# Kernel tuning notes

Measured on AMD Instinct MI355X. Metric: run time of the kernel, lower is better.

## Reference

```python
import jax, jax.numpy as jnp
import numpy as np

DIST_THRESH = 150.0
ROW_EPS = 1e-6
BN_EPS = 1e-5


def setup_inputs() -> dict:
    key = jax.random.key(0)
    ks = jax.random.split(key, 6)
    B, N, T, D = 64, 64, 16, 512
    person_features = jax.random.normal(ks[0], (B, N, T, D), dtype=jnp.float32)
    # bboxes in pixel-ish units so the 150px threshold gives a mixed adjacency
    bboxes = jax.random.uniform(ks[1], (B, N, 4), dtype=jnp.float32) * 300.0
    w1 = jax.random.normal(ks[2], (D, D), dtype=jnp.float32) * (1.0 / np.sqrt(D))
    b1 = jax.random.normal(ks[3], (D,), dtype=jnp.float32) * 0.02
    w2 = jax.random.normal(ks[4], (D, D), dtype=jnp.float32) * (1.0 / np.sqrt(D))
    b2 = jax.random.normal(ks[5], (D,), dtype=jnp.float32) * 0.02
    g1 = jnp.ones((D,), jnp.float32); beta1 = jnp.zeros((D,), jnp.float32)
    g2 = jnp.ones((D,), jnp.float32); beta2 = jnp.zeros((D,), jnp.float32)
    return {"person_features": person_features, "bboxes": bboxes,
            "w1": w1, "b1": b1, "g1": g1, "beta1": beta1,
            "w2": w2, "b2": b2, "g2": g2, "beta2": beta2}


def _build_adjacency(bboxes):
    # centers: (B, N, 2) from x+w/2, y+h/2
    cx = bboxes[..., 0] + 0.5 * bboxes[..., 2]
    cy = bboxes[..., 1] + 0.5 * bboxes[..., 3]
    centers = jnp.stack([cx, cy], axis=-1)
    # pairwise distances (B, N, N), vectorized (replaces B*N*N python loop)
    diff = centers[:, :, None, :] - centers[:, None, :, :]
    dist = jnp.sqrt(jnp.sum(diff * diff, axis=-1))
    N = bboxes.shape[1]
    eye = jnp.eye(N, dtype=bboxes.dtype)
    off_diag = (eye[None] == 0.0)
    A = jnp.where((dist < DIST_THRESH) & off_diag, 1.0, 0.0) + eye[None]
    return A


def _stgcn(x, A, w, b, g, beta):
    # x: (B, N, C); A: (B, N, N)
    # torch: A_norm = A / (A.sum(dim=1 of A[i] -> axis=2) + eps)
    A_norm = A / (jnp.sum(A, axis=2, keepdims=True) + ROW_EPS)
    # x_graph = x[b].T @ A_norm[b]  -> (B, C, N)
    y = jnp.einsum('bnc,bnm->bcm', x, A_norm)
    # 1x1 conv == channel GEMM, bias added per out-channel
    y = jnp.einsum('oc,bcm->bom', w, y) + b[None, :, None]
    # BatchNorm2d in training mode: biased stats over (batch, spatial)
    mean = jnp.mean(y, axis=(0, 2), keepdims=True)
    var = jnp.mean(jnp.square(y - mean), axis=(0, 2), keepdims=True)
    y = (y - mean) / jnp.sqrt(var + BN_EPS)
    y = y * g[None, :, None] + beta[None, :, None]
    y = jax.nn.relu(y)
    return jnp.swapaxes(y, 1, 2)  # (B, N, C)


def reference(person_features, bboxes, w1, b1, g1, beta1, w2, b2, g2, beta2):
    A = _build_adjacency(bboxes)
    x = person_features[:, :, -1, :]  # (B, N, D) last frame
    h = _stgcn(x, A, w1, b1, g1, beta1)
    h = _stgcn(h, A, w2, b2, g2, beta2)
    # write enhanced features back into last timestep
    return person_features.at[:, :, -1, :].set(h)
```

## Files before the change

kernel.cpp:

```cpp
#include <hip/hip_runtime.h>
#include <hip/hip_bf16.h>


typedef __attribute__((ext_vector_type(8))) short short8;
typedef __attribute__((ext_vector_type(4))) float v4f;

#define DIST_THRESH 150.0f
#define ROW_EPS 1e-6f
#define BN_EPS 1e-5f

__device__ __forceinline__ ushort f2bf(float f) {
  union { __hip_bfloat16 h; ushort u; } cv;
  cv.h = __float2bfloat16(f);
  return cv.u;
}

__global__ __launch_bounds__(64) void k_adj(const float* __restrict__ bb,
                                            float* __restrict__ An) {
  int b = blockIdx.x;
  int t = threadIdx.x;
  __shared__ float cx[64], cy[64];
  float4 v = *(const float4*)&bb[(size_t)(b * 64 + t) * 4];
  cx[t] = v.x + 0.5f * v.z;
  cy[t] = v.y + 0.5f * v.w;
  __syncthreads();
  float mycx = cx[t], mycy = cy[t];
  float rs = 0.f;
  for (int m = 0; m < 64; ++m) {
    float dx = mycx - cx[m], dy = mycy - cy[m];
    float d = sqrtf(dx * dx + dy * dy);
    float a = (m == t) ? 1.0f : ((d < DIST_THRESH) ? 1.0f : 0.0f);
    rs += a;
  }
  float inv = 1.0f / (rs + ROW_EPS);
  float* row = An + (size_t)b * 4096 + (size_t)t * 64;
  for (int m = 0; m < 64; ++m) {
    float dx = mycx - cx[m], dy = mycy - cy[m];
    float d = sqrtf(dx * dx + dy * dy);
    float a = (m == t) ? 1.0f : ((d < DIST_THRESH) ? 1.0f : 0.0f);
    row[m] = a * inv;
  }
}

__global__ __launch_bounds__(256) void k_prep(const float* __restrict__ w1,
                                              const float* __restrict__ w2,
                                              ushort* __restrict__ wb,
                                              float* __restrict__ stats) {
  int idx = blockIdx.x * 256 + threadIdx.x;
  float v = (idx < 262144) ? w1[idx] : w2[idx - 262144];
  wb[idx] = f2bf(v);
  if (idx < 2048) stats[idx] = 0.f;
}

__global__ __launch_bounds__(256) void k_copy(const float4* __restrict__ in,
                                              float4* __restrict__ out) {
  size_t i = (size_t)blockIdx.x * 256 + threadIdx.x;
#pragma unroll
  for (int j = 0; j < 4; ++j) {
    size_t idx = i + (size_t)j * 2097152;
    int tt = (int)((idx >> 7) & 15);
    if (tt != 15) out[idx] = in[idx];
  }
}

__global__ __launch_bounds__(256) void k_agg(const float* __restrict__ Xbase,
                                             int rowStride,
                                             const float* __restrict__ An,
                                             ushort* __restrict__ Z) {
  int b = blockIdx.x;
  int c0 = blockIdx.y * 128;
  __shared__ float Xs[64][128];
  __shared__ float As[64][64];
  int t = threadIdx.x;

  const float* xb = Xbase + (size_t)b * 64 * rowStride;
  for (int i = t; i < 2048; i += 256) {
    int n = i >> 5, c4 = (i & 31) << 2;
    *(float4*)&Xs[n][c4] = *(const float4*)&xb[(size_t)n * rowStride + c0 + c4];
  }
  const float4* ab = (const float4*)(An + (size_t)b * 4096);
  for (int i = t; i < 1024; i += 256) ((float4*)As)[i] = ab[i];
  __syncthreads();

  int c4 = (t & 31) << 2;
  int m0 = (t >> 5) << 3;
  float4 acc[8];
#pragma unroll
  for (int i = 0; i < 8; ++i) acc[i] = make_float4(0.f, 0.f, 0.f, 0.f);

  for (int n = 0; n < 64; ++n) {
    float4 x = *(const float4*)&Xs[n][c4];
    float4 a0 = *(const float4*)&As[n][m0];
    float4 a1 = *(const float4*)&As[n][m0 + 4];
    float as[8] = {a0.x, a0.y, a0.z, a0.w, a1.x, a1.y, a1.z, a1.w};
#pragma unroll
    for (int i = 0; i < 8; ++i) {
      acc[i].x = fmaf(as[i], x.x, acc[i].x);
      acc[i].y = fmaf(as[i], x.y, acc[i].y);
      acc[i].z = fmaf(as[i], x.z, acc[i].z);
      acc[i].w = fmaf(as[i], x.w, acc[i].w);
    }
  }

  size_t zbase = (size_t)b * 64 * 512 + c0 + c4;
#pragma unroll
  for (int i = 0; i < 8; ++i) {
    int m = m0 + i;
    ushort4 zz;
    zz.x = f2bf(acc[i].x);
    zz.y = f2bf(acc[i].y);
    zz.z = f2bf(acc[i].z);
    zz.w = f2bf(acc[i].w);
    *(ushort4*)&Z[zbase + (size_t)m * 512] = zz;
  }
}

__global__ __launch_bounds__(256) void k_gemm(const ushort* __restrict__ Z,
                                              const ushort* __restrict__ W,
                                              const float* __restrict__ bias,
                                              float* __restrict__ Y,
                                              float* __restrict__ sum,
                                              float* __restrict__ sumsq) {
  __shared__ __align__(16) ushort Zs[64 * 40];
  __shared__ __align__(16) ushort Ws[64 * 40];
  __shared__ float redS[4][64], redQ[4][64];

  int t = threadIdx.x;
  int r0 = blockIdx.x * 64;
  int o0 = blockIdx.y * 64;
  int wv = t >> 6, lane = t & 63;
  int m = lane & 15, q = lane >> 4;

  v4f acc[4];
#pragma unroll
  for (int nf = 0; nf < 4; ++nf) acc[nf] = (v4f){0.f, 0.f, 0.f, 0.f};

  int srow = t >> 2, scg = (t & 3) << 3;

  for (int ks = 0; ks < 16; ++ks) {
    int k0 = ks * 32;
    __syncthreads();
    uint4 zv = *(const uint4*)&Z[(size_t)(r0 + srow) * 512 + k0 + scg];
    uint4 wvv = *(const uint4*)&W[(size_t)(o0 + srow) * 512 + k0 + scg];
    *(uint4*)&Zs[srow * 40 + scg] = zv;
    *(uint4*)&Ws[srow * 40 + scg] = wvv;
    __syncthreads();

    short8 a = *(const short8*)&Zs[(wv * 16 + m) * 40 + q * 8];
#pragma unroll
    for (int nf = 0; nf < 4; ++nf) {
      short8 bfr = *(const short8*)&Ws[(nf * 16 + m) * 40 + q * 8];
      acc[nf] = __builtin_amdgcn_mfma_f32_16x16x32_bf16(a, bfr, acc[nf], 0, 0, 0);
    }
  }

#pragma unroll
  for (int nf = 0; nf < 4; ++nf) {
    int col = o0 + nf * 16 + m;
    float bv = bias[col];
    float s = 0.f, s2 = 0.f;
#pragma unroll
    for (int reg = 0; reg < 4; ++reg) {
      int row = r0 + wv * 16 + q * 4 + reg;
      float y = acc[nf][reg] + bv;
      Y[(size_t)row * 512 + col] = y;
      s += y;
      s2 += y * y;
    }
    s += __shfl_xor(s, 16);
    s += __shfl_xor(s, 32);
    s2 += __shfl_xor(s2, 16);
    s2 += __shfl_xor(s2, 32);
    if (q == 0) {
      redS[wv][nf * 16 + m] = s;
      redQ[wv][nf * 16 + m] = s2;
    }
  }
  __syncthreads();
  if (t < 64) {
    float s = redS[0][t] + redS[1][t] + redS[2][t] + redS[3][t];
    float s2 = redQ[0][t] + redQ[1][t] + redQ[2][t] + redQ[3][t];
    atomicAdd(&sum[o0 + t], s);
    atomicAdd(&sumsq[o0 + t], s2);
  }
}

__global__ __launch_bounds__(256) void k_norm(const float* __restrict__ Y,
                                              const float* __restrict__ sum,
                                              const float* __restrict__ sumsq,
                                              const float* __restrict__ g,
                                              const float* __restrict__ beta,
                                              float* __restrict__ out,
                                              int lastSlice) {
  int idx = blockIdx.x * 256 + threadIdx.x;
  int o = (idx & 127) << 2;
  int r = idx >> 7;
  float4 y = *(const float4*)&Y[(size_t)r * 512 + o];
  float4 sm = *(const float4*)&sum[o];
  float4 sq = *(const float4*)&sumsq[o];
  float4 gg = *(const float4*)&g[o];
  float4 bb = *(const float4*)&beta[o];
  const float inv = 1.0f / 4096.0f;
  float4 h;
  {
    float mean = sm.x * inv, var = sq.x * inv - mean * mean;
    h.x = fmaxf(gg.x * (y.x - mean) * rsqrtf(var + BN_EPS) + bb.x, 0.f);
  }
  {
    float mean = sm.y * inv, var = sq.y * inv - mean * mean;
    h.y = fmaxf(gg.y * (y.y - mean) * rsqrtf(var + BN_EPS) + bb.y, 0.f);
  }
  {
    float mean = sm.z * inv, var = sq.z * inv - mean * mean;
    h.z = fmaxf(gg.z * (y.z - mean) * rsqrtf(var + BN_EPS) + bb.z, 0.f);
  }
  {
    float mean = sm.w * inv, var = sq.w * inv - mean * mean;
    h.w = fmaxf(gg.w * (y.w - mean) * rsqrtf(var + BN_EPS) + bb.w, 0.f);
  }
  if (lastSlice)
    *(float4*)&out[((size_t)r * 16 + 15) * 512 + o] = h;
  else
    *(float4*)&out[(size_t)r * 512 + o] = h;
}

extern "C" void kernel_launch(void* const* d_in, const int* in_sizes, int n_in,
                              void* d_out, int out_size, void* d_ws, size_t ws_size,
                              hipStream_t stream) {
  const float* pf = (const float*)d_in[0];
  const float* bboxes = (const float*)d_in[1];
  const float* w1 = (const float*)d_in[2];
  const float* b1 = (const float*)d_in[3];
  const float* g1 = (const float*)d_in[4];
  const float* be1 = (const float*)d_in[5];
  const float* w2 = (const float*)d_in[6];
  const float* b2 = (const float*)d_in[7];
  const float* g2 = (const float*)d_in[8];
  const float* be2 = (const float*)d_in[9];
  float* out = (float*)d_out;

  float* An = (float*)d_ws;
  ushort* wb = (ushort*)(An + 262144);
  ushort* Zb = wb + 524288;
  float* Yb = (float*)(Zb + 2097152);
  float* H1 = Yb + 2097152;
  float* stats = H1 + 2097152;
  float* sum1 = stats;
  float* sq1 = stats + 512;
  float* sum2 = stats + 1024;
  float* sq2 = stats + 1536;

  k_adj<<<64, 64, 0, stream>>>(bboxes, An);
  k_prep<<<2048, 256, 0, stream>>>(w1, w2, wb, stats);
  k_copy<<<8192, 256, 0, stream>>>((const float4*)pf, (float4*)out);

  k_agg<<<dim3(64, 4), 256, 0, stream>>>(pf + 7680, 8192, An, Zb);
  k_gemm<<<dim3(64, 8), 256, 0, stream>>>(Zb, wb, b1, Yb, sum1, sq1);
  k_norm<<<2048, 256, 0, stream>>>(Yb, sum1, sq1, g1, be1, H1, 0);

  k_agg<<<dim3(64, 4), 256, 0, stream>>>(H1, 512, An, Zb);
  k_gemm<<<dim3(64, 8), 256, 0, stream>>>(Zb, wb + 262144, b2, Yb, sum2, sq2);
  k_norm<<<2048, 256, 0, stream>>>(Yb, sum2, sq2, g2, be2, out, 1);
}
```

Before: 327.1 us.

## Fuse adjacency, first BN+ReLU, and prep kernels into the aggregation and copy kernels

The weight-prep and stats-zeroing kernel is merged into the bulk copy kernel as extra blocks. The adjacency build moves into each aggregation block, so the normalized adjacency buffer is gone. The first layer's BatchNorm+ReLU is now applied on the fly when the second aggregation loads Y, so one normalization pass and the H1 intermediate buffer are dropped. This saves launches and about one read/write pass over an 8 MB tensor. In exchange, every aggregation block repeats the serial 64x64 distance computation on only 64 threads before its main loop.

```diff
diff --git a/kernel.cpp b/kernel.cpp
--- a/kernel.cpp
+++ b/kernel.cpp
@@ -15,71 +15,100 @@
   return cv.u;
 }
 
-__global__ __launch_bounds__(64) void k_adj(const float* __restrict__ bb,
-                                            float* __restrict__ An) {
-  int b = blockIdx.x;
+__global__ __launch_bounds__(256) void k_copy_prep(const float4* __restrict__ in,
+                                                   float4* __restrict__ out,
+                                                   const float* __restrict__ w1,
+                                                   const float* __restrict__ w2,
+                                                   ushort* __restrict__ wb,
+                                                   float* __restrict__ stats) {
+  int blk = blockIdx.x;
   int t = threadIdx.x;
-  __shared__ float cx[64], cy[64];
-  float4 v = *(const float4*)&bb[(size_t)(b * 64 + t) * 4];
-  cx[t] = v.x + 0.5f * v.z;
-  cy[t] = v.y + 0.5f * v.w;
-  __syncthreads();
-  float mycx = cx[t], mycy = cy[t];
-  float rs = 0.f;
-  for (int m = 0; m < 64; ++m) {
-    float dx = mycx - cx[m], dy = mycy - cy[m];
-    float d = sqrtf(dx * dx + dy * dy);
-    float a = (m == t) ? 1.0f : ((d < DIST_THRESH) ? 1.0f : 0.0f);
-    rs += a;
-  }
-  float inv = 1.0f / (rs + ROW_EPS);
-  float* row = An + (size_t)b * 4096 + (size_t)t * 64;
-  for (int m = 0; m < 64; ++m) {
-    float dx = mycx - cx[m], dy = mycy - cy[m];
-    float d = sqrtf(dx * dx + dy * dy);
-    float a = (m == t) ? 1.0f : ((d < DIST_THRESH) ? 1.0f : 0.0f);
-    row[m] = a * inv;
-  }
-}
-
-__global__ __launch_bounds__(256) void k_prep(const float* __restrict__ w1,
-                                              const float* __restrict__ w2,
-                                              ushort* __restrict__ wb,
-                                              float* __restrict__ stats) {
-  int idx = blockIdx.x * 256 + threadIdx.x;
-  float v = (idx < 262144) ? w1[idx] : w2[idx - 262144];
-  wb[idx] = f2bf(v);
-  if (idx < 2048) stats[idx] = 0.f;
-}
-
-__global__ __launch_bounds__(256) void k_copy(const float4* __restrict__ in,
-                                              float4* __restrict__ out) {
-  size_t i = (size_t)blockIdx.x * 256 + threadIdx.x;
-#pragma unroll
-  for (int j = 0; j < 4; ++j) {
-    size_t idx = i + (size_t)j * 2097152;
-    int tt = (int)((idx >> 7) & 15);
-    if (tt != 15) out[idx] = in[idx];
+  if (blk < 8192) {
+    size_t i = (size_t)blk * 256 + t;
+#pragma unroll
+    for (int j = 0; j < 4; ++j) {
+      size_t idx = i + (size_t)j * 2097152;
+      int tt = (int)((idx >> 7) & 15);
+      if (tt != 15) out[idx] = in[idx];
+    }
+  } else {
+    int idx = (blk - 8192) * 256 + t;
+    float v = (idx < 262144) ? w1[idx] : w2[idx - 262144];
+    wb[idx] = f2bf(v);
+    if (idx < 2048) stats[idx] = 0.f;
   }
 }
 
 __global__ __launch_bounds__(256) void k_agg(const float* __restrict__ Xbase,
                                              int rowStride,
-                                             const float* __restrict__ An,
+                                             const float* __restrict__ bb,
+                                             const float* __restrict__ stats,
+                                             const float* __restrict__ g,
+                                             const float* __restrict__ beta,
+                                             int applyBN,
                                              ushort* __restrict__ Z) {
   int b = blockIdx.x;
   int c0 = blockIdx.y * 128;
+  int t = threadIdx.x;
   __shared__ float Xs[64][128];
   __shared__ float As[64][64];
-  int t = threadIdx.x;
+  __shared__ float cxs[64], cys[64];
+  __shared__ float scaleS[128], shiftS[128];
+
+  if (t < 64) {
+    float4 v = *(const float4*)&bb[(size_t)(b * 64 + t) * 4];
+    cxs[t] = v.x + 0.5f * v.z;
+    cys[t] = v.y + 0.5f * v.w;
+  }
+  if (applyBN && t < 32) {
+    int c = t * 4;
+    float4 sm = *(const float4*)&stats[c0 + c];
+    float4 sq = *(const float4*)&stats[512 + c0 + c];
+    float4 gg = *(const float4*)&g[c0 + c];
+    float4 bt = *(const float4*)&beta[c0 + c];
+    const float inv = 1.0f / 4096.0f;
+    float mean, var, sc;
+    mean = sm.x * inv; var = sq.x * inv - mean * mean; sc = gg.x * rsqrtf(var + BN_EPS);
+    scaleS[c] = sc; shiftS[c] = bt.x - mean * sc;
+    mean = sm.y * inv; var = sq.y * inv - mean * mean; sc = gg.y * rsqrtf(var + BN_EPS);
+    scaleS[c + 1] = sc; shiftS[c + 1] = bt.y - mean * sc;
+    mean = sm.z * inv; var = sq.z * inv - mean * mean; sc = gg.z * rsqrtf(var + BN_EPS);
+    scaleS[c + 2] = sc; shiftS[c + 2] = bt.z - mean * sc;
+    mean = sm.w * inv; var = sq.w * inv - mean * mean; sc = gg.w * rsqrtf(var + BN_EPS);
+    scaleS[c + 3] = sc; shiftS[c + 3] = bt.w - mean * sc;
+  }
+  __syncthreads();
+
+  if (t < 64) {
+    float mycx = cxs[t], mycy = cys[t];
+    float rs = 0.f;
+    for (int m = 0; m < 64; ++m) {
+      float dx = mycx - cxs[m], dy = mycy - cys[m];
+      float d = sqrtf(dx * dx + dy * dy);
+      float a = (m == t) ? 1.0f : ((d < DIST_THRESH) ? 1.0f : 0.0f);
+      rs += a;
+    }
+    float inv = 1.0f / (rs + ROW_EPS);
+    for (int m = 0; m < 64; ++m) {
+      float dx = mycx - cxs[m], dy = mycy - cys[m];
+      float d = sqrtf(dx * dx + dy * dy);
+      float a = (m == t) ? 1.0f : ((d < DIST_THRESH) ? 1.0f : 0.0f);
+      As[t][m] = a * inv;
+    }
+  }
 
   const float* xb = Xbase + (size_t)b * 64 * rowStride;
   for (int i = t; i < 2048; i += 256) {
     int n = i >> 5, c4 = (i & 31) << 2;
-    *(float4*)&Xs[n][c4] = *(const float4*)&xb[(size_t)n * rowStride + c0 + c4];
-  }
-  const float4* ab = (const float4*)(An + (size_t)b * 4096);
-  for (int i = t; i < 1024; i += 256) ((float4*)As)[i] = ab[i];
+    float4 x = *(const float4*)&xb[(size_t)n * rowStride + c0 + c4];
+    if (applyBN) {
+      x.x = fmaxf(x.x * scaleS[c4] + shiftS[c4], 0.f);
+      x.y = fmaxf(x.y * scaleS[c4 + 1] + shiftS[c4 + 1], 0.f);
+      x.z = fmaxf(x.z * scaleS[c4 + 2] + shiftS[c4 + 2], 0.f);
+      x.w = fmaxf(x.w * scaleS[c4 + 3] + shiftS[c4 + 3], 0.f);
+    }
+    *(float4*)&Xs[n][c4] = x;
+  }
   __syncthreads();
 
   int c4 = (t & 31) << 2;
@@ -190,8 +219,7 @@
                                               const float* __restrict__ sumsq,
                                               const float* __restrict__ g,
                                               const float* __restrict__ beta,
-                                              float* __restrict__ out,
-                                              int lastSlice) {
+                                              float* __restrict__ out) {
   int idx = blockIdx.x * 256 + threadIdx.x;
   int o = (idx & 127) << 2;
   int r = idx >> 7;
@@ -218,10 +246,7 @@
     float mean = sm.w * inv, var = sq.w * inv - mean * mean;
     h.w = fmaxf(gg.w * (y.w - mean) * rsqrtf(var + BN_EPS) + bb.w, 0.f);
   }
-  if (lastSlice)
-    *(float4*)&out[((size_t)r * 16 + 15) * 512 + o] = h;
-  else
-    *(float4*)&out[(size_t)r * 512 + o] = h;
+  *(float4*)&out[((size_t)r * 16 + 15) * 512 + o] = h;
 }
 
 extern "C" void kernel_launch(void* const* d_in, const int* in_sizes, int n_in,
@@ -239,26 +264,22 @@
   const float* be2 = (const float*)d_in[9];
   float* out = (float*)d_out;
 
-  float* An = (float*)d_ws;
-  ushort* wb = (ushort*)(An + 262144);
+  ushort* wb = (ushort*)d_ws;
   ushort* Zb = wb + 524288;
   float* Yb = (float*)(Zb + 2097152);
-  float* H1 = Yb + 2097152;
-  float* stats = H1 + 2097152;
+  float* stats = Yb + 2097152;
   float* sum1 = stats;
   float* sq1 = stats + 512;
   float* sum2 = stats + 1024;
   float* sq2 = stats + 1536;
 
-  k_adj<<<64, 64, 0, stream>>>(bboxes, An);
-  k_prep<<<2048, 256, 0, stream>>>(w1, w2, wb, stats);
-  k_copy<<<8192, 256, 0, stream>>>((const float4*)pf, (float4*)out);
-
-  k_agg<<<dim3(64, 4), 256, 0, stream>>>(pf + 7680, 8192, An, Zb);
+  k_copy_prep<<<10240, 256, 0, stream>>>((const float4*)pf, (float4*)out, w1, w2, wb, stats);
+
+  k_agg<<<dim3(64, 4), 256, 0, stream>>>(pf + 7680, 8192, bboxes, stats, g1, be1, 0, Zb);
   k_gemm<<<dim3(64, 8), 256, 0, stream>>>(Zb, wb, b1, Yb, sum1, sq1);
-  k_norm<<<2048, 256, 0, stream>>>(Yb, sum1, sq1, g1, be1, H1, 0);
-
-  k_agg<<<dim3(64, 4), 256, 0, stream>>>(H1, 512, An, Zb);
+
+  k_agg<<<dim3(64, 4), 256, 0, stream>>>(Yb, 512, bboxes, stats, g1, be1, 1, Zb);
   k_gemm<<<dim3(64, 8), 256, 0, stream>>>(Zb, wb + 262144, b2, Yb, sum2, sq2);
-  k_norm<<<2048, 256, 0, stream>>>(Yb, sum2, sq2, g2, be2, out, 1);
-}
+
+  k_norm<<<2048, 256, 0, stream>>>(Yb, sum2, sq2, g2, be2, out);
+}
```

New measurement: 318.6 us. -2.6%, faster.
